# Optimization experiments

Measured on AMD Instinct MI355X. Metric: run time of the kernel, lower is better.

Reference implementation:

```python
import jax, jax.numpy as jnp
import numpy as np

N = 2048
BS = N // 2  # rotations per block


def _round_robin_blocks(n: int) -> np.ndarray:
    """Circle-method round-robin pairing; n assumed even. Shape (n-1, n//2, 2)."""
    seq = list(range(n))
    blocks = []
    for _ in range(n - 1):
        first = seq[: n // 2]
        second = seq[n // 2:][::-1]
        blocks.append(list(zip(first, second)))
        rest = seq[1:]
        seq = [seq[0]] + [rest[-1]] + rest[:-1]  # deque.rotate(1)
    return np.asarray(blocks, dtype=np.int64)


def setup_inputs() -> dict:
    key = jax.random.key(0)
    k1, k2 = jax.random.split(key)
    x = jax.random.normal(k1, (8192, N), dtype=jnp.float32)
    angles = jax.random.normal(k2, (N * (N - 1) // 2,), dtype=jnp.float32)
    bias = jnp.zeros((N,), dtype=jnp.float32)
    blocks = jnp.asarray(_round_robin_blocks(N))  # (N-1, N//2, 2) int64 indices
    return {"x": x, "angles": angles, "bias": bias, "blocks": blocks}


def _build_rotation(angles, blocks):
    """Sequentially apply n-1 blocks of parallel Givens rotations to columns of eye(n)."""
    ang_per_block = angles.reshape(N - 1, BS)  # block b uses angles[b*BS : (b+1)*BS]

    def step(U, inp):
        ang, blk = inp
        i_idx, j_idx = blk[:, 0], blk[:, 1]
        c = jnp.cos(ang)[None, :]  # (1, BS)
        s = jnp.sin(ang)[None, :]
        ui = U[:, i_idx]  # (N, BS)
        uj = U[:, j_idx]
        U = U.at[:, i_idx].set(c * ui + s * uj)
        U = U.at[:, j_idx].set(-s * ui + c * uj)
        return U, None

    U0 = jnp.eye(N, dtype=angles.dtype)
    U, _ = jax.lax.scan(step, U0, (ang_per_block, blocks))
    return U


def reference(x, angles, bias, blocks):
    U = _build_rotation(angles, blocks)
    # einsum '... i, o i -> ... o'  ==  x @ U.T
    return jnp.einsum("bi,oi->bo", x, U) + bias
```

## Files before the change

### kernel.cpp

```cpp
#include <hip/hip_runtime.h>
#include <hip/hip_bf16.h>

#define NN      2048
#define NSTEPS  2047
#define MROWS   8192
#define PADK    8

typedef __attribute__((ext_vector_type(8))) __bf16 bf16x8;
typedef __attribute__((ext_vector_type(4))) float  f32x4;
typedef __attribute__((ext_vector_type(2))) float  f32x2;

struct LeafOuts { unsigned short* p[8]; };

__device__ __forceinline__ unsigned short f2bf(float f) {
  unsigned int u = __float_as_uint(f);
  u += 0x7fffu + ((u >> 16) & 1u);
  return (unsigned short)(u >> 16);
}

__device__ __forceinline__ void gload_lds16(const void* g, void* l) {
  __builtin_amdgcn_global_load_lds((const __attribute__((address_space(1))) void*)g,
                                   (__attribute__((address_space(3))) void*)l, 16, 0, 0);
}

template<int CTRL>
__device__ __forceinline__ float dppf(float v) {
  return __int_as_float(__builtin_amdgcn_update_dpp(
      __float_as_int(v), __float_as_int(v), CTRL, 0xf, 0xf, false));
}
#define DPP_UP 0x138
#define DPP_DN 0x130

__device__ __forceinline__ f32x2 pk_smul(f32x2 cs, f32x2 v) {
  f32x2 d;
  asm("v_pk_mul_f32 %0, %1, %2 op_sel:[1,0] op_sel_hi:[1,1]"
      : "=v"(d) : "v"(cs), "v"(v));
  return d;
}
__device__ __forceinline__ f32x2 pk_cfma(f32x2 cs, f32x2 v, f32x2 a) {
  f32x2 d;
  asm("v_pk_fma_f32 %0, %1, %2, %3 op_sel:[0,0,0] op_sel_hi:[0,1,1]"
      : "=v"(d) : "v"(cs), "v"(v), "v"(a));
  return d;
}
__device__ __forceinline__ f32x2 pk_cfma_neg(f32x2 cs, f32x2 v, f32x2 a) {
  f32x2 d;
  asm("v_pk_fma_f32 %0, %1, %2, %3 op_sel:[0,0,0] op_sel_hi:[0,1,1] neg_lo:[0,0,1] neg_hi:[0,0,1]"
      : "=v"(d) : "v"(cs), "v"(v), "v"(a));
  return d;
}

__global__ __launch_bounds__(256) void prep_kernel(
    const float* __restrict__ angles, float2* __restrict__ cs) {
  int t = blockIdx.x * 256 + threadIdx.x;
  if (t >= NSTEPS * 1024) return;
  const int slice = t >> 10;
  const int w     = t & 1023;
  const int plane = w >> 8;
  const int r     = w & 255;
  const int entry = r >> 1;
  const int b     = r & 1;
  const int p     = 8 * entry + 2 * plane + b;
  float s, c;
  sincosf(angles[slice * 1024 + p], &s, &c);
  cs[t] = make_float2(c, s);
}

__global__ __launch_bounds__(256) void cvt_kernel(
    const float4* __restrict__ x, ushort4* __restrict__ xb, int n4) {
  int idx = blockIdx.x * 256 + threadIdx.x;
  if (idx >= n4) return;
  float4 v = x[idx];
  ushort4 o;
  o.x = f2bf(v.x); o.y = f2bf(v.y); o.z = f2bf(v.z); o.w = f2bf(v.w);
  xb[idx] = o;
}

__global__ __launch_bounds__(256) void zero_kernel(uint4* __restrict__ p, int n) {
  int idx = blockIdx.x * 256 + threadIdx.x;
  const int stride = gridDim.x * 256;
  const uint4 z = make_uint4(0, 0, 0, 0);
  for (; idx < n; idx += stride) p[idx] = z;
}

template<int LC>
__global__ __launch_bounds__(256) void leaf_kernel(
    const char* __restrict__ csb, LeafOuts outs, int c_base, int first_rm,
    int cmask, int cshift) {
  const int tid  = threadIdx.x;
  const int lane = tid & 63;
  const int cl   = blockIdx.x & cmask;
  const int v    = ((blockIdx.x >> cshift) << 2) + (tid >> 6);
  const int c    = c_base + cl;
  const int t0   = 254 * c;
  unsigned short* out = outs.p[cl];
  const bool rm = (first_rm != 0) && (cl == 0);

  const int pA = 2 * v, pB = 2 * v + 1;
  const int kA = (pA <= 1023) ? pA : 2047 - pA;
  const int kBp = (pB <= 1023) ? pB : 2047 - pB;
  const int kmin = min(kA, kBp);
  int kb = (kmin - 254) & ~1;
  kb = min(max(kb, 0), 512);
  const bool l0 = (lane == 0), l63 = (lane == 63);
  const bool c0l0  = (kb == 0)   && l0;
  const bool cTl63 = (kb == 512) && l63;

  f32x2 FF[8], SS[8];
#pragma unroll
  for (int e = 0; e < 8; ++e) {
    const int k = kb + 8 * lane + e, m = 2047 - k;
    FF[e] = (f32x2){(k == pA) ? 1.f : 0.f, (k == pB) ? 1.f : 0.f};
    SS[e] = (f32x2){(m == pA) ? 1.f : 0.f, (m == pB) ? 1.f : 0.f};
  }

  const int kb8 = kb >> 3, mm = (kb >> 1) & 3;
  const char* base = csb + (size_t)t0 * 8192 + 16 * lane;
  const char* gE[4];
  const char* gO[4];
#pragma unroll
  for (int ep = 0; ep < 4; ++ep) {
    const int u = mm + ep;
    const int off = (u & 3) * 2048 + (kb8 + (u >> 2)) * 16;
    gE[ep] = base + off;
    gO[ep] = base + off + 8192;
  }
  float4 cE0 = *(const float4*)gE[0], cE1 = *(const float4*)gE[1];
  float4 cE2 = *(const float4*)gE[2], cE3 = *(const float4*)gE[3];
  float4 cO0 = *(const float4*)gO[0], cO1 = *(const float4*)gO[1];
  float4 cO2 = *(const float4*)gO[2], cO3 = *(const float4*)gO[3];
#pragma unroll
  for (int ep = 0; ep < 4; ++ep) { gE[ep] += 16384; gO[ep] += 16384; }

#define CP(CV, K) (((const f32x2*)&(CV))[(K)])

#define ROTE(E, CPp) { \
    const int rF = ((E) - PHI) & 7, rS = ((E) + PHI) & 7; \
    const f32x2 cp_ = (CPp); \
    const f32x2 t_ = pk_smul(cp_, SS[rS]); \
    const f32x2 u_ = pk_smul(cp_, FF[rF]); \
    FF[rF] = pk_cfma(cp_, FF[rF], t_); \
    SS[rS] = pk_cfma_neg(cp_, SS[rS], u_); }

#define LSTEP(PHI_, C0, C1, C2, C3, GP) { \
    const int PHI = (PHI_); \
    const int pF = (7 - PHI) & 7, pT = (8 - PHI) & 7; \
    ROTE(0, CP(C0, 0)) ROTE(1, CP(C0, 1)) \
    ROTE(2, CP(C1, 0)) ROTE(3, CP(C1, 1)) \
    ROTE(4, CP(C2, 0)) ROTE(5, CP(C2, 1)) \
    ROTE(6, CP(C3, 0)) ROTE(7, CP(C3, 1)) \
    const f32x2 Fo = FF[pF], So = SS[PHI], St = FF[pT]; \
    f32x2 fi, sd; \
    fi.x = dppf<DPP_UP>(Fo.x); fi.y = dppf<DPP_UP>(Fo.y); \
    sd.x = dppf<DPP_DN>(So.x); sd.y = dppf<DPP_DN>(So.y); \
    C0 = *(const float4*)GP[0]; C1 = *(const float4*)GP[1]; \
    C2 = *(const float4*)GP[2]; C3 = *(const float4*)GP[3]; \
    GP[0] += 16384; GP[1] += 16384; GP[2] += 16384; GP[3] += 16384; \
    const f32x2 z2 = {0.f, 0.f}; \
    const f32x2 xF = c0l0 ? St : z2; \
    const f32x2 xS = cTl63 ? Fo : z2; \
    FF[pF]  = l0  ? xF : fi; \
    SS[PHI] = l63 ? xS : sd; \
    FF[pT]  = c0l0 ? So : FF[pT]; \
  }

  constexpr int ITERS = LC / 8;
  constexpr int TAIL  = LC & 7;
#pragma unroll 1
  for (int it = 0; it < ITERS; ++it) {
    LSTEP(0, cE0, cE1, cE2, cE3, gE)
    LSTEP(1, cO0, cO1, cO2, cO3, gO)
    LSTEP(2, cE0, cE1, cE2, cE3, gE)
    LSTEP(3, cO0, cO1, cO2, cO3, gO)
    LSTEP(4, cE0, cE1, cE2, cE3, gE)
    LSTEP(5, cO0, cO1, cO2, cO3, gO)
    LSTEP(6, cE0, cE1, cE2, cE3, gE)
    LSTEP(7, cO0, cO1, cO2, cO3, gO)
  }
  if constexpr (TAIL >= 1) LSTEP(0, cE0, cE1, cE2, cE3, gE)
  if constexpr (TAIL >= 2) LSTEP(1, cO0, cO1, cO2, cO3, gO)
  if constexpr (TAIL >= 3) LSTEP(2, cE0, cE1, cE2, cE3, gE)
  if constexpr (TAIL >= 4) LSTEP(3, cO0, cO1, cO2, cO3, gO)
  if constexpr (TAIL >= 5) LSTEP(4, cE0, cE1, cE2, cE3, gE)
  if constexpr (TAIL >= 6) LSTEP(5, cO0, cO1, cO2, cO3, gO)
  if constexpr (TAIL >= 7) LSTEP(6, cE0, cE1, cE2, cE3, gE)

  constexpr int RPH = LC & 7;
  const int tend = t0 + LC;
  const int rA = (pA == 0) ? 0 : ((pA - 1 - t0 + 4094) % 2047) + 1;
  const int rB = ((pB - 1 - t0 + 4094) % 2047) + 1;
#pragma unroll
  for (int e = 0; e < 8; ++e) {
    const int k = kb + 8 * lane + e;
    const int lF = (k == 0) ? 0 : ((k - 1 - tend + 4094) % 2047) + 1;
    const int lS = ((2046 - k - tend + 4094) % 2047) + 1;
    const f32x2 fv = FF[(e - RPH) & 7];
    const f32x2 sv = SS[(e + RPH) & 7];
    if (rm) {
      out[(size_t)rA * NN + lF] = f2bf(fv.x);
      out[(size_t)rB * NN + lF] = f2bf(fv.y);
      out[(size_t)rA * NN + lS] = f2bf(sv.x);
      out[(size_t)rB * NN + lS] = f2bf(sv.y);
    } else {
      out[(size_t)lF * NN + rA] = f2bf(fv.x);
      out[(size_t)lF * NN + rB] = f2bf(fv.y);
      out[(size_t)lS * NN + rA] = f2bf(sv.x);
      out[(size_t)lS * NN + rB] = f2bf(sv.y);
    }
  }
}

__device__ __forceinline__ void arc_kr(int a, int len, int& lo, int& hi) {
  int last = a + len - 1; if (last > 2047) last -= 2047;
  const int k1 = min(a, 2047 - a), k2 = min(last, 2047 - last);
  lo = min(k1, k2); hi = max(k1, k2);
  int d;
  d = 1023 - a; if (d < 0) d += 2047; if (d < len) hi = 1023;
  d = 1024 - a; if (d < 0) d += 2047; if (d < len) hi = 1023;
  d = 2047 - a; if (d < 0) d += 2047; if (d < len) lo = 0;
  d = 1    - a; if (d < 0) d += 2047; if (d < len) lo = min(lo, 1);
}

#define BM 128
#define BN 128
#define BK 32

__global__ __launch_bounds__(256) void comp_kernel(
    const unsigned short* __restrict__ A, const unsigned short* __restrict__ B,
    unsigned short* __restrict__ C, int ta, int tb) {
  __shared__ unsigned short As[BM * BK];
  __shared__ unsigned short Bs[BN * BK];
  const int tid  = threadIdx.x;
  const int lane = tid & 63;
  const int wave = tid >> 6;
  const int bm = blockIdx.x, bn = blockIdx.y;
  const int wm = wave & 1, wn = wave >> 1;

  const int n0 = bn * BN;
  int qlo, qhi;
  {
    const int nfirst = (n0 == 0) ? 1 : n0;
    const int a = ((nfirst - 1 + tb) % 2047) + 1;
    const int len = (n0 == 0) ? (BN - 1) : BN;
    arc_kr(a, len, qlo, qhi);
    if (n0 == 0) qlo = 0;
  }
  const int L = tb - ta;
  const int KAc = max(qlo - L - PADK, 0);
  const int KBc = min(qhi + L + PADK, 1023);

  const int srow = wave * 16 + (lane >> 2);
  const int scol = (lane & 3) * 8;
  const unsigned short* Ag = A + (size_t)(bm * BM + srow) * NN + scol;
  const unsigned short* Bg = B + (size_t)(bn * BN + srow) * NN + scol;

  const int fm = lane & 15;
  const int kbr = lane >> 4;

  f32x4 acc[4][4];
#pragma unroll
  for (int a_ = 0; a_ < 4; ++a_)
#pragma unroll
    for (int b_ = 0; b_ < 4; ++b_) acc[a_][b_] = (f32x4){0.f, 0.f, 0.f, 0.f};

  for (int kt = 0; kt < NN / BK; ++kt) {
    const int k0 = kt * BK;
    {
      const int kfirst = (k0 == 0) ? 1 : k0;
      const int a2 = ((kfirst - 1 + ta) % 2047) + 1;
      const int len2 = (k0 == 0) ? (BK - 1) : BK;
      int tlo, thi; arc_kr(a2, len2, tlo, thi);
      if (k0 == 0) tlo = 0;
      if (thi < KAc || tlo > KBc) continue;
    }
#pragma unroll
    for (int it = 0; it < 2; ++it) {
      gload_lds16(Ag + (size_t)(it * 64) * NN + k0, &As[wave * 512 + it * 2048]);
      gload_lds16(Bg + (size_t)(it * 64) * NN + k0, &Bs[wave * 512 + it * 2048]);
    }
    __syncthreads();

    bf16x8 af[4], bfr[4];
#pragma unroll
    for (int a_ = 0; a_ < 4; ++a_)
      af[a_] = *(const bf16x8*)&As[(wm * 64 + a_ * 16 + fm) * BK + kbr * 8];
#pragma unroll
    for (int b_ = 0; b_ < 4; ++b_)
      bfr[b_] = *(const bf16x8*)&Bs[(wn * 64 + b_ * 16 + fm) * BK + kbr * 8];
#pragma unroll
    for (int a_ = 0; a_ < 4; ++a_)
#pragma unroll
      for (int b_ = 0; b_ < 4; ++b_)
        acc[a_][b_] = __builtin_amdgcn_mfma_f32_16x16x32_bf16(af[a_], bfr[b_], acc[a_][b_], 0, 0, 0);
    __syncthreads();
  }

  const int row_in = (lane >> 4) * 4;
#pragma unroll
  for (int a_ = 0; a_ < 4; ++a_) {
#pragma unroll
    for (int b_ = 0; b_ < 4; ++b_) {
      const int gn = bn * BN + wn * 64 + b_ * 16 + fm;
#pragma unroll
      for (int v = 0; v < 4; ++v) {
        const int gm = bm * BM + wm * 64 + a_ * 16 + row_in + v;
        C[(size_t)gm * NN + gn] = f2bf(acc[a_][b_][v]);
      }
    }
  }
}

__global__ __launch_bounds__(256) void gemm_kernel(
    const unsigned short* __restrict__ A, const unsigned short* __restrict__ B,
    const float* __restrict__ bias, float* __restrict__ C) {
  __shared__ unsigned short As[BM * BK];
  __shared__ unsigned short Bs[BN * BK];
  const int tid  = threadIdx.x;
  const int lane = tid & 63;
  const int wave = tid >> 6;
  const int bm = blockIdx.x, bn = blockIdx.y;
  const int wm = wave & 1, wn = wave >> 1;

  const int srow = wave * 16 + (lane >> 2);
  const int scol = (lane & 3) * 8;
  const unsigned short* Ag = A + (size_t)(bm * BM + srow) * NN + scol;
  const unsigned short* Bg = B + (size_t)(bn * BN + srow) * NN + scol;

  const int fm = lane & 15;
  const int kbr = lane >> 4;

  f32x4 acc[4][4];
#pragma unroll
  for (int a_ = 0; a_ < 4; ++a_)
#pragma unroll
    for (int b_ = 0; b_ < 4; ++b_) acc[a_][b_] = (f32x4){0.f, 0.f, 0.f, 0.f};

  for (int kt = 0; kt < NN / BK; ++kt) {
    const int k0 = kt * BK;
#pragma unroll
    for (int it = 0; it < 2; ++it) {
      gload_lds16(Ag + (size_t)(it * 64) * NN + k0, &As[wave * 512 + it * 2048]);
      gload_lds16(Bg + (size_t)(it * 64) * NN + k0, &Bs[wave * 512 + it * 2048]);
    }
    __syncthreads();

    bf16x8 af[4], bfr[4];
#pragma unroll
    for (int a_ = 0; a_ < 4; ++a_)
      af[a_] = *(const bf16x8*)&As[(wm * 64 + a_ * 16 + fm) * BK + kbr * 8];
#pragma unroll
    for (int b_ = 0; b_ < 4; ++b_)
      bfr[b_] = *(const bf16x8*)&Bs[(wn * 64 + b_ * 16 + fm) * BK + kbr * 8];
#pragma unroll
    for (int a_ = 0; a_ < 4; ++a_)
#pragma unroll
      for (int b_ = 0; b_ < 4; ++b_)
        acc[a_][b_] = __builtin_amdgcn_mfma_f32_16x16x32_bf16(af[a_], bfr[b_], acc[a_][b_], 0, 0, 0);
    __syncthreads();
  }

  const int row_in = (lane >> 4) * 4;
#pragma unroll
  for (int a_ = 0; a_ < 4; ++a_) {
#pragma unroll
    for (int b_ = 0; b_ < 4; ++b_) {
      const int gn = bn * BN + wn * 64 + b_ * 16 + fm;
      const float bv = bias[gn];
#pragma unroll
      for (int v = 0; v < 4; ++v) {
        const int gm = bm * BM + wm * 64 + a_ * 16 + row_in + v;
        C[(size_t)gm * NN + gn] = acc[a_][b_][v] + bv;
      }
    }
  }
}

extern "C" void kernel_launch(void* const* d_in, const int* in_sizes, int n_in,
                              void* d_out, int out_size, void* d_ws, size_t ws_size,
                              hipStream_t stream) {
  const float* x      = (const float*)d_in[0];
  const float* angles = (const float*)d_in[1];
  const float* bias   = (const float*)d_in[2];
  float* out = (float*)d_out;

  char* ws = (char*)d_ws;
  unsigned short* P0  = (unsigned short*)(ws + 0);
  unsigned short* P1  = (unsigned short*)(ws + 8388608);
  char*           cs  = ws + 16777216;
  unsigned short* B7  = (unsigned short*)(ws + 33587200);
  unsigned short* B8  = (unsigned short*)(ws + 41975808);
  unsigned short* xb  = (unsigned short*)(ws + 16777216);

  char* ob = (char*)d_out;
  unsigned short* B1 = (unsigned short*)(ob + 0);
  unsigned short* B2 = (unsigned short*)(ob + 8388608);
  unsigned short* B3 = (unsigned short*)(ob + 16777216);
  unsigned short* B4 = (unsigned short*)(ob + 25165824);
  unsigned short* B5 = (unsigned short*)(ob + 33554432);
  unsigned short* B6 = (unsigned short*)(ob + 41943040);

  prep_kernel<<<dim3(8188), dim3(256), 0, stream>>>(angles, (float2*)cs);
  zero_kernel<<<dim3(2048), dim3(256), 0, stream>>>((uint4*)ob, 50331648 / 16);
  zero_kernel<<<dim3(1024), dim3(256), 0, stream>>>((uint4*)P0, 8388608 / 16);
  zero_kernel<<<dim3(1024), dim3(256), 0, stream>>>((uint4*)(ws + 33587200), 16777216 / 16);

  LeafOuts lo_main;
  lo_main.p[0] = P0; lo_main.p[1] = B1; lo_main.p[2] = B2; lo_main.p[3] = B3;
  lo_main.p[4] = B4; lo_main.p[5] = B5; lo_main.p[6] = B6; lo_main.p[7] = B7;
  leaf_kernel<254><<<dim3(2048), dim3(256), 0, stream>>>(cs, lo_main, 0, 1, 7, 3);
  LeafOuts lo_tail;
  for (int i = 0; i < 8; ++i) lo_tail.p[i] = B8;
  leaf_kernel<15><<<dim3(256), dim3(256), 0, stream>>>(cs, lo_tail, 8, 0, 0, 0);

  comp_kernel<<<dim3(16, 16), dim3(256), 0, stream>>>(P0, B1, P1,  254,  508);
  comp_kernel<<<dim3(16, 16), dim3(256), 0, stream>>>(P1, B2, P0,  508,  762);
  comp_kernel<<<dim3(16, 16), dim3(256), 0, stream>>>(P0, B3, P1,  762, 1016);
  comp_kernel<<<dim3(16, 16), dim3(256), 0, stream>>>(P1, B4, P0, 1016, 1270);
  comp_kernel<<<dim3(16, 16), dim3(256), 0, stream>>>(P0, B5, P1, 1270, 1524);
  comp_kernel<<<dim3(16, 16), dim3(256), 0, stream>>>(P1, B6, P0, 1524, 1778);
  comp_kernel<<<dim3(16, 16), dim3(256), 0, stream>>>(P0, B7, P1, 1778, 2032);
  comp_kernel<<<dim3(16, 16), dim3(256), 0, stream>>>(P1, B8, P0, 2032, 2047);

  cvt_kernel<<<dim3(16384), dim3(256), 0, stream>>>((const float4*)x, (ushort4*)xb,
                                                    MROWS * NN / 4);
  gemm_kernel<<<dim3(MROWS / BM, NN / BN), dim3(256), 0, stream>>>(xb, P0, bias, out);
}
```

Baseline: 842.5 us.

## Run early rotation steps on a narrower 256-wide window before widening to 512

For the 254-step chunk, the kernel now runs the first 124 steps with 4 elements per lane (a 256-wide window), because the nonzero support of the basis vectors is still small then. It then redistributes the state into the 8-per-lane layout with cross-lane shuffles and finishes the remaining 130 steps in the original wide path. This is meant to cut the rotation arithmetic and coefficient loads in the early phase. The cost is extra shuffle work at the transition and more complex window-boundary logic, which risks correctness if the support grows beyond the narrow window.

```diff
diff --git a/kernel.cpp b/kernel.cpp
--- a/kernel.cpp
+++ b/kernel.cpp
@@ -107,30 +107,6 @@
   const bool cTl63 = (kb == 512) && l63;
 
   f32x2 FF[8], SS[8];
-#pragma unroll
-  for (int e = 0; e < 8; ++e) {
-    const int k = kb + 8 * lane + e, m = 2047 - k;
-    FF[e] = (f32x2){(k == pA) ? 1.f : 0.f, (k == pB) ? 1.f : 0.f};
-    SS[e] = (f32x2){(m == pA) ? 1.f : 0.f, (m == pB) ? 1.f : 0.f};
-  }
-
-  const int kb8 = kb >> 3, mm = (kb >> 1) & 3;
-  const char* base = csb + (size_t)t0 * 8192 + 16 * lane;
-  const char* gE[4];
-  const char* gO[4];
-#pragma unroll
-  for (int ep = 0; ep < 4; ++ep) {
-    const int u = mm + ep;
-    const int off = (u & 3) * 2048 + (kb8 + (u >> 2)) * 16;
-    gE[ep] = base + off;
-    gO[ep] = base + off + 8192;
-  }
-  float4 cE0 = *(const float4*)gE[0], cE1 = *(const float4*)gE[1];
-  float4 cE2 = *(const float4*)gE[2], cE3 = *(const float4*)gE[3];
-  float4 cO0 = *(const float4*)gO[0], cO1 = *(const float4*)gO[1];
-  float4 cO2 = *(const float4*)gO[2], cO3 = *(const float4*)gO[3];
-#pragma unroll
-  for (int ep = 0; ep < 4; ++ep) { gE[ep] += 16384; gO[ep] += 16384; }
 
 #define CP(CV, K) (((const f32x2*)&(CV))[(K)])
 
@@ -164,26 +140,188 @@
     FF[pT]  = c0l0 ? So : FF[pT]; \
   }
 
-  constexpr int ITERS = LC / 8;
-  constexpr int TAIL  = LC & 7;
+  if constexpr (LC == 254) {
+    const int kb2 = min(max((kmin - 124) & ~1, 0), 768);
+    const bool a0l0  = (kb2 == 0)   && l0;
+    const bool aTl63 = (kb2 == 768) && l63;
+
+#pragma unroll
+    for (int e = 0; e < 4; ++e) {
+      const int k = kb2 + 4 * lane + e, m = 2047 - k;
+      FF[e] = (f32x2){(k == pA) ? 1.f : 0.f, (k == pB) ? 1.f : 0.f};
+      SS[e] = (f32x2){(m == pA) ? 1.f : 0.f, (m == pB) ? 1.f : 0.f};
+    }
+
+    const int ub = (kb2 >> 1) + 2 * lane;
+    const char* csq = csb + (size_t)t0 * 8192;
+    const char* aE0 = csq + ((ub & 3) * 2048 + (ub >> 2) * 16);
+    const char* aE1 = csq + ((((ub + 1) & 3)) * 2048 + ((ub + 1) >> 2) * 16);
+    const char* aO0 = aE0 + 8192;
+    const char* aO1 = aE1 + 8192;
+    float4 A0E = *(const float4*)aE0, A1E = *(const float4*)aE1;
+    float4 A0O = *(const float4*)aO0, A1O = *(const float4*)aO1;
+    aE0 += 16384; aE1 += 16384; aO0 += 16384; aO1 += 16384;
+
+#define ROTE4(E, CPp) { \
+    const int rF = ((E) - PHI) & 3, rS = ((E) + PHI) & 3; \
+    const f32x2 cp_ = (CPp); \
+    const f32x2 t_ = pk_smul(cp_, SS[rS]); \
+    const f32x2 u_ = pk_smul(cp_, FF[rF]); \
+    FF[rF] = pk_cfma(cp_, FF[rF], t_); \
+    SS[rS] = pk_cfma_neg(cp_, SS[rS], u_); }
+
+#define ASTEP(PHI_, C0, C1, GP0, GP1) { \
+    const int PHI = (PHI_); \
+    const int pF = (3 - PHI) & 3, pT = (4 - PHI) & 3; \
+    ROTE4(0, CP(C0, 0)) ROTE4(1, CP(C0, 1)) \
+    ROTE4(2, CP(C1, 0)) ROTE4(3, CP(C1, 1)) \
+    const f32x2 Fo = FF[pF], So = SS[PHI], St = FF[pT]; \
+    f32x2 fi, sd; \
+    fi.x = dppf<DPP_UP>(Fo.x); fi.y = dppf<DPP_UP>(Fo.y); \
+    sd.x = dppf<DPP_DN>(So.x); sd.y = dppf<DPP_DN>(So.y); \
+    C0 = *(const float4*)GP0; C1 = *(const float4*)GP1; \
+    GP0 += 16384; GP1 += 16384; \
+    const f32x2 z2 = {0.f, 0.f}; \
+    const f32x2 xF = a0l0 ? St : z2; \
+    const f32x2 xS = aTl63 ? Fo : z2; \
+    FF[pF]  = l0  ? xF : fi; \
+    SS[PHI] = l63 ? xS : sd; \
+    FF[pT]  = a0l0 ? So : FF[pT]; \
+  }
+
 #pragma unroll 1
-  for (int it = 0; it < ITERS; ++it) {
+    for (int it = 0; it < 31; ++it) {
+      ASTEP(0, A0E, A1E, aE0, aE1)
+      ASTEP(1, A0O, A1O, aO0, aO1)
+      ASTEP(2, A0E, A1E, aE0, aE1)
+      ASTEP(3, A0O, A1O, aO0, aO1)
+    }
+
+    {
+      const int dlt = kb2 - kb;
+      const int base_d = 8 * lane - dlt;
+      f32x2 nF[8], nS[8];
+
+#define TGETF(E, SR) { \
+      const int d_ = base_d + (E); \
+      const int sl_ = (d_ >> 2) & 63; \
+      f32x2 fv_; \
+      fv_.x = __shfl(FF[SR].x, sl_); \
+      fv_.y = __shfl(FF[SR].y, sl_); \
+      nF[E] = ((unsigned)d_ < 256u) ? fv_ : (f32x2){0.f, 0.f}; }
+#define TGETS(E, SR) { \
+      const int d_ = base_d + (E); \
+      const int sl_ = (d_ >> 2) & 63; \
+      f32x2 sv_; \
+      sv_.x = __shfl(SS[SR].x, sl_); \
+      sv_.y = __shfl(SS[SR].y, sl_); \
+      nS[E] = ((unsigned)d_ < 256u) ? sv_ : (f32x2){0.f, 0.f}; }
+
+      if ((dlt & 3) == 0) {
+        TGETF(0,0) TGETF(1,1) TGETF(2,2) TGETF(3,3)
+        TGETF(4,0) TGETF(5,1) TGETF(6,2) TGETF(7,3)
+      } else {
+        TGETF(0,2) TGETF(1,3) TGETF(2,0) TGETF(3,1)
+        TGETF(4,2) TGETF(5,3) TGETF(6,0) TGETF(7,1)
+      }
+      FF[4] = nF[0]; FF[5] = nF[1]; FF[6] = nF[2]; FF[7] = nF[3];
+      FF[0] = nF[4]; FF[1] = nF[5]; FF[2] = nF[6]; FF[3] = nF[7];
+      if ((dlt & 3) == 0) {
+        TGETS(0,0) TGETS(1,1) TGETS(2,2) TGETS(3,3)
+        TGETS(4,0) TGETS(5,1) TGETS(6,2) TGETS(7,3)
+      } else {
+        TGETS(0,2) TGETS(1,3) TGETS(2,0) TGETS(3,1)
+        TGETS(4,2) TGETS(5,3) TGETS(6,0) TGETS(7,1)
+      }
+      SS[4] = nS[0]; SS[5] = nS[1]; SS[6] = nS[2]; SS[7] = nS[3];
+      SS[0] = nS[4]; SS[1] = nS[5]; SS[2] = nS[6]; SS[3] = nS[7];
+    }
+
+    const int kb8 = kb >> 3, mm = (kb >> 1) & 3;
+    const char* basep = csb + (size_t)t0 * 8192 + 16 * lane + (size_t)124 * 8192;
+    const char* gE[4];
+    const char* gO[4];
+#pragma unroll
+    for (int ep = 0; ep < 4; ++ep) {
+      const int u = mm + ep;
+      const int off = (u & 3) * 2048 + (kb8 + (u >> 2)) * 16;
+      gE[ep] = basep + off;
+      gO[ep] = basep + off + 8192;
+    }
+    float4 cE0 = *(const float4*)gE[0], cE1 = *(const float4*)gE[1];
+    float4 cE2 = *(const float4*)gE[2], cE3 = *(const float4*)gE[3];
+    float4 cO0 = *(const float4*)gO[0], cO1 = *(const float4*)gO[1];
+    float4 cO2 = *(const float4*)gO[2], cO3 = *(const float4*)gO[3];
+#pragma unroll
+    for (int ep = 0; ep < 4; ++ep) { gE[ep] += 16384; gO[ep] += 16384; }
+
+    LSTEP(4, cE0, cE1, cE2, cE3, gE)
+    LSTEP(5, cO0, cO1, cO2, cO3, gO)
+    LSTEP(6, cE0, cE1, cE2, cE3, gE)
+    LSTEP(7, cO0, cO1, cO2, cO3, gO)
+#pragma unroll 1
+    for (int it = 0; it < 15; ++it) {
+      LSTEP(0, cE0, cE1, cE2, cE3, gE)
+      LSTEP(1, cO0, cO1, cO2, cO3, gO)
+      LSTEP(2, cE0, cE1, cE2, cE3, gE)
+      LSTEP(3, cO0, cO1, cO2, cO3, gO)
+      LSTEP(4, cE0, cE1, cE2, cE3, gE)
+      LSTEP(5, cO0, cO1, cO2, cO3, gO)
+      LSTEP(6, cE0, cE1, cE2, cE3, gE)
+      LSTEP(7, cO0, cO1, cO2, cO3, gO)
+    }
     LSTEP(0, cE0, cE1, cE2, cE3, gE)
     LSTEP(1, cO0, cO1, cO2, cO3, gO)
     LSTEP(2, cE0, cE1, cE2, cE3, gE)
     LSTEP(3, cO0, cO1, cO2, cO3, gO)
     LSTEP(4, cE0, cE1, cE2, cE3, gE)
     LSTEP(5, cO0, cO1, cO2, cO3, gO)
-    LSTEP(6, cE0, cE1, cE2, cE3, gE)
-    LSTEP(7, cO0, cO1, cO2, cO3, gO)
-  }
-  if constexpr (TAIL >= 1) LSTEP(0, cE0, cE1, cE2, cE3, gE)
-  if constexpr (TAIL >= 2) LSTEP(1, cO0, cO1, cO2, cO3, gO)
-  if constexpr (TAIL >= 3) LSTEP(2, cE0, cE1, cE2, cE3, gE)
-  if constexpr (TAIL >= 4) LSTEP(3, cO0, cO1, cO2, cO3, gO)
-  if constexpr (TAIL >= 5) LSTEP(4, cE0, cE1, cE2, cE3, gE)
-  if constexpr (TAIL >= 6) LSTEP(5, cO0, cO1, cO2, cO3, gO)
-  if constexpr (TAIL >= 7) LSTEP(6, cE0, cE1, cE2, cE3, gE)
+  } else {
+#pragma unroll
+    for (int e = 0; e < 8; ++e) {
+      const int k = kb + 8 * lane + e, m = 2047 - k;
+      FF[e] = (f32x2){(k == pA) ? 1.f : 0.f, (k == pB) ? 1.f : 0.f};
+      SS[e] = (f32x2){(m == pA) ? 1.f : 0.f, (m == pB) ? 1.f : 0.f};
+    }
+    const int kb8 = kb >> 3, mm = (kb >> 1) & 3;
+    const char* basep = csb + (size_t)t0 * 8192 + 16 * lane;
+    const char* gE[4];
+    const char* gO[4];
+#pragma unroll
+    for (int ep = 0; ep < 4; ++ep) {
+      const int u = mm + ep;
+      const int off = (u & 3) * 2048 + (kb8 + (u >> 2)) * 16;
+      gE[ep] = basep + off;
+      gO[ep] = basep + off + 8192;
+    }
+    float4 cE0 = *(const float4*)gE[0], cE1 = *(const float4*)gE[1];
+    float4 cE2 = *(const float4*)gE[2], cE3 = *(const float4*)gE[3];
+    float4 cO0 = *(const float4*)gO[0], cO1 = *(const float4*)gO[1];
+    float4 cO2 = *(const float4*)gO[2], cO3 = *(const float4*)gO[3];
+#pragma unroll
+    for (int ep = 0; ep < 4; ++ep) { gE[ep] += 16384; gO[ep] += 16384; }
+
+    constexpr int ITERS = LC / 8;
+    constexpr int TAIL  = LC & 7;
+#pragma unroll 1
+    for (int it = 0; it < ITERS; ++it) {
+      LSTEP(0, cE0, cE1, cE2, cE3, gE)
+      LSTEP(1, cO0, cO1, cO2, cO3, gO)
+      LSTEP(2, cE0, cE1, cE2, cE3, gE)
+      LSTEP(3, cO0, cO1, cO2, cO3, gO)
+      LSTEP(4, cE0, cE1, cE2, cE3, gE)
+      LSTEP(5, cO0, cO1, cO2, cO3, gO)
+      LSTEP(6, cE0, cE1, cE2, cE3, gE)
+      LSTEP(7, cO0, cO1, cO2, cO3, gO)
+    }
+    if constexpr (TAIL >= 1) LSTEP(0, cE0, cE1, cE2, cE3, gE)
+    if constexpr (TAIL >= 2) LSTEP(1, cO0, cO1, cO2, cO3, gO)
+    if constexpr (TAIL >= 3) LSTEP(2, cE0, cE1, cE2, cE3, gE)
+    if constexpr (TAIL >= 4) LSTEP(3, cO0, cO1, cO2, cO3, gO)
+    if constexpr (TAIL >= 5) LSTEP(4, cE0, cE1, cE2, cE3, gE)
+    if constexpr (TAIL >= 6) LSTEP(5, cO0, cO1, cO2, cO3, gO)
+    if constexpr (TAIL >= 7) LSTEP(6, cE0, cE1, cE2, cE3, gE)
+  }
 
   constexpr int RPH = LC & 7;
   const int tend = t0 + LC;
```

After: 798.9 us. 5.2% less time.
